# Optimization experiments

Hardware: AMD Instinct MI355X
Metric: run time of the kernel (lower is better)

The kernel has to match this reference:

```python
import jax, jax.numpy as jnp
import numpy as np

DIM = 2048
NUM_HEADS = 16
HEAD_DIM = DIM // NUM_HEADS
ROPE_BASE = 10000.0


def _rotate_half(t):
    t1, t2 = jnp.split(t, 2, axis=-1)
    return jnp.concatenate([-t2, t1], axis=-1)


def _rope_sin_cos(seq_len):
    # fp32 angles, matching RoPE1D
    inv_freq = 1.0 / (ROPE_BASE ** (jnp.arange(0, HEAD_DIM, 2, dtype=jnp.float32) / HEAD_DIM))
    freqs = jnp.arange(seq_len, dtype=jnp.float32)[:, None] * inv_freq[None, :]  # [S, hd/2]
    angles = jnp.concatenate([freqs, freqs], axis=-1)  # [S, hd]
    return jnp.sin(angles), jnp.cos(angles)


def setup_inputs() -> dict:
    key = jax.random.key(0)
    ks = jax.random.split(key, 5)
    B, S = 2, 2048
    x = jax.random.normal(ks[0], (B, S, DIM), dtype=jnp.float32)
    scale = 1.0 / np.sqrt(DIM)
    W_qkv = jax.random.normal(ks[1], (DIM, 3 * DIM), dtype=jnp.float32) * scale
    b_qkv = jnp.zeros((3 * DIM,), dtype=jnp.float32)
    W_proj = jax.random.normal(ks[2], (DIM, DIM), dtype=jnp.float32) * scale
    b_proj = jnp.zeros((DIM,), dtype=jnp.float32)
    return {"x": x, "W_qkv": W_qkv, "b_qkv": b_qkv, "W_proj": W_proj, "b_proj": b_proj}


def reference(x, W_qkv, b_qkv, W_proj, b_proj):
    B, S, D = x.shape
    H, hd = NUM_HEADS, HEAD_DIM
    qkv = x @ W_qkv + b_qkv  # [B, S, 3D]
    qkv = qkv.reshape(B, S, 3, H, hd)
    q, k, v = qkv[:, :, 0], qkv[:, :, 1], qkv[:, :, 2]  # [B, S, H, hd]
    q, k, v = (t.transpose(0, 2, 1, 3) for t in (q, k, v))  # [B, H, S, hd]
    sin, cos = _rope_sin_cos(S)  # [S, hd]
    sin = sin[None, None]
    cos = cos[None, None]
    q = q * cos + _rotate_half(q) * sin
    k = k * cos + _rotate_half(k) * sin
    # scaled dot-product attention (non-causal, no mask, no dropout)
    scale = 1.0 / np.sqrt(hd).astype(np.float32)
    scores = jnp.einsum("bhqd,bhkd->bhqk", q, k) * scale
    attn = jax.nn.softmax(scores, axis=-1)
    out = jnp.einsum("bhqk,bhkd->bhqd", attn, v)  # [B, H, S, hd]
    out = out.transpose(0, 2, 1, 3).reshape(B, S, D)
    return out @ W_proj + b_proj
```

## Files before the change

### kernel.cpp

```cpp
#include <hip/hip_runtime.h>


typedef __attribute__((ext_vector_type(4))) float  f32x4;
typedef __attribute__((ext_vector_type(8))) short  short8;
typedef __attribute__((ext_vector_type(4))) float  fv4;
typedef __attribute__((ext_vector_type(4))) unsigned short us4;

#define MFMA16(accv, av, bv) \
  asm volatile("v_mfma_f32_16x16x32_bf16 %0, %1, %2, %0" : "+v"(accv) : "v"(av), "v"(bv))

__device__ __forceinline__ unsigned short f2bf(float f) {
  unsigned int u = __float_as_uint(f);
  u += 0x7fffu + ((u >> 16) & 1u);
  return (unsigned short)(u >> 16);
}

__device__ __forceinline__ void gl_lds16(const void* g, void* l) {
  __builtin_amdgcn_global_load_lds((const __attribute__((address_space(1))) void*)g,
                                   (__attribute__((address_space(3))) void*)l, 16, 0, 0);
}

__global__ void cvt_f32_bf16(const float* __restrict__ in,
                             unsigned short* __restrict__ out, int n4) {
  int i = blockIdx.x * blockDim.x + threadIdx.x;
  int stride = gridDim.x * blockDim.x;
  for (; i < n4; i += stride) {
    fv4 v = ((const fv4*)in)[i];
    us4 o;
    o[0] = f2bf(v[0]); o[1] = f2bf(v[1]); o[2] = f2bf(v[2]); o[3] = f2bf(v[3]);
    ((us4*)out)[i] = o;
  }
}

__global__ void transpose_cvt(const float* __restrict__ in,
                              unsigned short* __restrict__ out, int R, int C) {
  __shared__ float tile[32][33];
  int c0 = blockIdx.x * 32, r0 = blockIdx.y * 32;
  int tx = threadIdx.x, ty = threadIdx.y;
#pragma unroll
  for (int i = 0; i < 4; i++)
    tile[ty + i * 8][tx] = in[(size_t)(r0 + ty + i * 8) * C + c0 + tx];
  __syncthreads();
#pragma unroll
  for (int i = 0; i < 4; i++)
    out[(size_t)(c0 + ty + i * 8) * R + r0 + tx] = f2bf(tile[tx][ty + i * 8]);
}

__global__ __launch_bounds__(512, 2) void qkv_gemm(
    const unsigned short* __restrict__ A,
    const unsigned short* __restrict__ Bt,
    const float* __restrict__ bias,
    unsigned short* __restrict__ Qo,
    unsigned short* __restrict__ Ko,
    unsigned short* __restrict__ Vo)
{
  __shared__ __align__(16) unsigned short SH[65536];

  const int NWG = 384;
  int bid = blockIdx.x;
  int nid = (bid & 7) * (NWG / 8) + (bid >> 3);
  int by = nid / 24, bx = nid - by * 24;

  int tid = threadIdx.x;
  int wv = tid >> 6, lane = tid & 63;
  int wr = wv >> 2, wc = wv & 3;
  int g = lane >> 4, c = lane & 15;

  int m0 = by * 256, n0 = bx * 256;

  int lh = wc >> 1, jj = wc & 1;
  int F[4];
#pragma unroll
  for (int n = 0; n < 4; n++) F[n] = 8 * lh + 2 * jj + (n & 1) + ((n >> 1) << 2);

  f32x4 acc[8][4];
#pragma unroll
  for (int m = 0; m < 8; m++)
#pragma unroll
    for (int n = 0; n < 4; n++)
#pragma unroll
      for (int r = 0; r < 4; r++) acc[m][n][r] = 0.f;

  auto stage = [&](int buf, int kt) {
    int k0 = kt * 32;
    unsigned short* Ad = SH + buf * 8192;
    unsigned short* Bd = SH + 32768 + buf * 8192;
#pragma unroll
    for (int p = 0; p < 2; p++) {
      int e = p * 512 + tid;
      int row = e >> 2, sl = (e & 3) ^ ((row >> 1) & 3);
      gl_lds16(A  + (size_t)(m0 + row) * 2048 + k0 + sl * 8,
               Ad + p * 4096 + wv * 512);
      gl_lds16(Bt + (size_t)(n0 + row) * 2048 + k0 + sl * 8,
               Bd + p * 4096 + wv * 512);
    }
  };

  stage(0, 0); stage(1, 1); stage(2, 2);

  for (int t = 0; t < 64; t++) {
    if (t < 62)       asm volatile("s_waitcnt vmcnt(8)" ::: "memory");
    else if (t == 62) asm volatile("s_waitcnt vmcnt(4)" ::: "memory");
    else              asm volatile("s_waitcnt vmcnt(0)" ::: "memory");
    __builtin_amdgcn_s_barrier();

    const unsigned short* Ab = SH + (t & 3) * 8192;
    const unsigned short* Bb = SH + 32768 + (t & 3) * 8192;

    short8 af[8], bfv[4];
#pragma unroll
    for (int m = 0; m < 8; m++) {
      int row = wr * 128 + m * 16 + c;
      af[m] = *(const short8*)(Ab + row * 32 + ((g ^ ((row >> 1) & 3)) << 3));
    }
#pragma unroll
    for (int n = 0; n < 4; n++) {
      int row = F[n] * 16 + c;
      bfv[n] = *(const short8*)(Bb + row * 32 + ((g ^ ((row >> 1) & 3)) << 3));
    }

    if (t < 61) stage((t + 3) & 3, t + 3);

    __builtin_amdgcn_s_setprio(1);
#pragma unroll
    for (int m = 0; m < 8; m++)
#pragma unroll
      for (int n = 0; n < 4; n++)
        MFMA16(acc[m][n], af[m], bfv[n]);
    __builtin_amdgcn_s_setprio(0);
  }

  int sel = bx >> 3;
  int bxl = bx & 7;
  int b = by >> 3;

  float biasv[4];
#pragma unroll
  for (int n = 0; n < 4; n++) biasv[n] = bias[n0 + F[n] * 16 + c];

  if (sel == 2) {
    __syncthreads();
    unsigned short* Vs = SH;
#pragma unroll
    for (int m = 0; m < 8; m++)
#pragma unroll
      for (int n = 0; n < 4; n++) {
        int dp = F[n] * 16 + c;
        int sb = wr * 128 + m * 16 + 4 * g;
        us4 pk;
#pragma unroll
        for (int r = 0; r < 4; r++) pk[r] = f2bf(acc[m][n][r] + biasv[n]);
        *(us4*)(Vs + dp * 256 + (sb ^ ((dp & 7) << 3))) = pk;
      }
    __syncthreads();
#pragma unroll
    for (int it = 0; it < 16; it++) {
      int u = it * 512 + tid;
      int dp = u >> 5, ch = u & 31;
      short8 val = *(const short8*)(Vs + dp * 256 + ((ch ^ (dp & 7)) << 3));
      int head = bxl * 2 + (dp >> 7), d = dp & 127;
      int sg = (by & 7) * 256 + ch * 8;
      *(short8*)(Vo + ((size_t)((b * 16 + head) * 128 + d)) * 2048 + sg) = val;
    }
  } else {
    unsigned short* outp = (sel == 0) ? Qo : Ko;
    float qscale = (sel == 0) ? (0.08838834764831845f * 1.44269504088896340736f) : 1.0f;
    int head = bxl * 2 + lh;
    float invf[2];
#pragma unroll
    for (int j = 0; j < 2; j++)
      invf[j] = __expf(-(float)((2 * jj + j) * 16 + c) * 0.14391156831212787f);
#pragma unroll
    for (int m = 0; m < 8; m++) {
#pragma unroll
      for (int j = 0; j < 2; j++) {
        int dlo = (2 * jj + j) * 16 + c;
#pragma unroll
        for (int r = 0; r < 4; r++) {
          int s_seq = (by & 7) * 256 + wr * 128 + m * 16 + 4 * g + r;
          float ang = (float)s_seq * invf[j];
          float sn, cs;
          __sincosf(ang, &sn, &cs);
          float vlo = acc[m][j][r]     + biasv[j];
          float vhi = acc[m][j + 2][r] + biasv[j + 2];
          float rlo = (vlo * cs - vhi * sn) * qscale;
          float rhi = (vhi * cs + vlo * sn) * qscale;
          size_t base = ((size_t)((b * 16 + head) * 2048 + s_seq)) * 128;
          outp[base + dlo]      = f2bf(rlo);
          outp[base + dlo + 64] = f2bf(rhi);
        }
      }
    }
  }
}

__global__ __launch_bounds__(256, 2) void attn_kernel(
    const unsigned short* __restrict__ Qi,
    const unsigned short* __restrict__ Ki,
    const unsigned short* __restrict__ Vi,
    unsigned short* __restrict__ X2)
{
  __shared__ __align__(16) unsigned short Kl[2][64 * 128];
  __shared__ __align__(16) unsigned short Vl[2][128 * 64];
  __shared__ __align__(16) unsigned short Pl[4][32 * 64];

  int bid = blockIdx.x;
  int nid = (bid & 7) * 64 + (bid >> 3);
  int bh = nid >> 4, qblk = nid & 15;
  int tid = threadIdx.x, wv = tid >> 6, lane = tid & 63;
  int g = lane >> 4, c = lane & 15;

  const unsigned short* Kg = Ki + (size_t)bh * 2048 * 128;
  const unsigned short* Vg = Vi + (size_t)bh * 128 * 2048;
  const unsigned short* Qb = Qi + ((size_t)bh * 2048 + qblk * 128 + wv * 32) * 128;

  short8 qf[2][4];
#pragma unroll
  for (int qt = 0; qt < 2; qt++)
#pragma unroll
    for (int dc = 0; dc < 4; dc++)
      qf[qt][dc] = *(const short8*)(Qb + (size_t)(qt * 16 + c) * 128 + dc * 32 + g * 8);

  f32x4 accO[2][8];
#pragma unroll
  for (int qt = 0; qt < 2; qt++)
#pragma unroll
    for (int nt = 0; nt < 8; nt++)
#pragma unroll
      for (int r = 0; r < 4; r++) accO[qt][nt][r] = 0.f;
  float m_run[2] = {-3.0e38f, -3.0e38f};
  float l_run[2] = {0.f, 0.f};

  auto stage = [&](int bsel, int t0) {
#pragma unroll
    for (int j = 0; j < 4; j++) {
      int e = j * 256 + tid;
      int s = e >> 4, sl = e & 15;
      gl_lds16(Kg + (size_t)(t0 + s) * 128 + ((sl ^ (s & 7)) * 8),
               &Kl[bsel][(size_t)(j * 256 + wv * 64) * 8]);
    }
#pragma unroll
    for (int j = 0; j < 4; j++) {
      int e = j * 256 + tid;
      int d = e >> 3, sl = e & 7;
      gl_lds16(Vg + (size_t)d * 2048 + t0 + ((sl ^ (d & 7)) * 8),
               &Vl[bsel][(size_t)(j * 256 + wv * 64) * 8]);
    }
  };

  stage(0, 0);
  __syncthreads();

  int cur = 0;
  for (int t = 0; t < 32; t++) {
    if (t < 31) stage(cur ^ 1, (t + 1) * 64);

    const unsigned short* Kt_ = &Kl[cur][0];
    const unsigned short* Vt_ = &Vl[cur][0];
    unsigned short* Pw = &Pl[wv][0];

    f32x4 sc[2][4];
#pragma unroll
    for (int qt = 0; qt < 2; qt++)
#pragma unroll
      for (int kt = 0; kt < 4; kt++)
#pragma unroll
        for (int r = 0; r < 4; r++) sc[qt][kt][r] = 0.f;

#pragma unroll
    for (int kt = 0; kt < 4; kt++) {
      short8 kf[4];
#pragma unroll
      for (int dc = 0; dc < 4; dc++)
        kf[dc] = *(const short8*)(Kt_ + (size_t)(kt * 16 + c) * 128 +
                                  (((dc * 4 + g) ^ (c & 7)) * 8));
      __builtin_amdgcn_s_setprio(1);
#pragma unroll
      for (int dc = 0; dc < 4; dc++) {
        MFMA16(sc[0][kt], kf[dc], qf[0][dc]);
        MFMA16(sc[1][kt], kf[dc], qf[1][dc]);
      }
      __builtin_amdgcn_s_setprio(0);
    }

    float mx[2];
#pragma unroll
    for (int qt = 0; qt < 2; qt++) {
      f32x4 mv = sc[qt][0];
#pragma unroll
      for (int kt = 1; kt < 4; kt++)
#pragma unroll
        for (int r = 0; r < 4; r++) mv[r] = fmaxf(mv[r], sc[qt][kt][r]);
      float m0 = fmaxf(fmaxf(mv[0], mv[1]), fmaxf(mv[2], mv[3]));
      m0 = fmaxf(m0, __shfl_xor(m0, 16));
      m0 = fmaxf(m0, __shfl_xor(m0, 32));
      mx[qt] = m0;
    }
    if (__any((mx[0] > m_run[0]) || (mx[1] > m_run[1]))) {
#pragma unroll
      for (int qt = 0; qt < 2; qt++) {
        float mnew = fmaxf(m_run[qt], mx[qt]);
        float al = __builtin_exp2f(m_run[qt] - mnew);
        l_run[qt] *= al;
        m_run[qt] = mnew;
#pragma unroll
        for (int r = 0; r < 4; r++) {
          float alr = __shfl(al, 4 * g + r);
#pragma unroll
          for (int nt = 0; nt < 8; nt++) accO[qt][nt][r] *= alr;
        }
      }
    }
#pragma unroll
    for (int qt = 0; qt < 2; qt++) {
      float rs = 0.f;
#pragma unroll
      for (int kt = 0; kt < 4; kt++) {
        float p0 = __builtin_exp2f(sc[qt][kt][0] - m_run[qt]);
        float p1 = __builtin_exp2f(sc[qt][kt][1] - m_run[qt]);
        float p2 = __builtin_exp2f(sc[qt][kt][2] - m_run[qt]);
        float p3 = __builtin_exp2f(sc[qt][kt][3] - m_run[qt]);
        rs += (p0 + p1) + (p2 + p3);
        unsigned int lo, hi;
        asm("v_cvt_pk_bf16_f32 %0, %1, %2" : "=v"(lo) : "v"(p0), "v"(p1));
        asm("v_cvt_pk_bf16_f32 %0, %1, %2" : "=v"(hi) : "v"(p2), "v"(p3));
        uint2 pk; pk.x = lo; pk.y = hi;
        *(uint2*)(Pw + (size_t)(qt * 16 + c) * 64 +
                  (((kt * 2 + (g >> 1)) ^ (c & 7)) * 8) + (g & 1) * 4) = pk;
      }
      rs += __shfl_xor(rs, 16);
      rs += __shfl_xor(rs, 32);
      l_run[qt] += rs;
    }

    short8 pa[2][2];
#pragma unroll
    for (int qt = 0; qt < 2; qt++)
#pragma unroll
      for (int kc = 0; kc < 2; kc++)
        pa[qt][kc] = *(const short8*)(Pw + (size_t)(qt * 16 + c) * 64 +
                                      (((kc * 4 + g) ^ (c & 7)) * 8));
#pragma unroll
    for (int nt = 0; nt < 8; nt++) {
      short8 vf0 = *(const short8*)(Vt_ + (size_t)(nt * 16 + c) * 64 +
                                    ((g ^ (c & 7)) * 8));
      short8 vf1 = *(const short8*)(Vt_ + (size_t)(nt * 16 + c) * 64 +
                                    (((4 + g) ^ (c & 7)) * 8));
      __builtin_amdgcn_s_setprio(1);
      MFMA16(accO[0][nt], pa[0][0], vf0);
      MFMA16(accO[1][nt], pa[1][0], vf0);
      MFMA16(accO[0][nt], pa[0][1], vf1);
      MFMA16(accO[1][nt], pa[1][1], vf1);
      __builtin_amdgcn_s_setprio(0);
    }

    __syncthreads();
    cur ^= 1;
  }

  float rl[2] = {1.f / l_run[0], 1.f / l_run[1]};
  int b = bh >> 4, h = bh & 15;
  size_t rowbase = (size_t)b * 2048 + qblk * 128 + wv * 32;
#pragma unroll
  for (int qt = 0; qt < 2; qt++)
#pragma unroll
    for (int r = 0; r < 4; r++) {
      float rr = __shfl(rl[qt], 4 * g + r);
      size_t row = rowbase + qt * 16 + 4 * g + r;
#pragma unroll
      for (int nt = 0; nt < 8; nt++)
        X2[row * 2048 + h * 128 + nt * 16 + c] = f2bf(accO[qt][nt][r] * rr);
    }
}

__global__ __launch_bounds__(512, 2) void proj_gemm(
    const unsigned short* __restrict__ A,
    const unsigned short* __restrict__ Bt,
    const float* __restrict__ bias,
    float* __restrict__ Co)
{
  __shared__ __align__(16) unsigned short SH[49152];

  int bid = blockIdx.x;
  int nid = (bid & 7) * 32 + (bid >> 3);
  int by = nid >> 4, bx = nid & 15;

  int tid = threadIdx.x;
  int wv = tid >> 6, lane = tid & 63;
  int wr = wv >> 1, wc = wv & 1;
  int g = lane >> 4, c = lane & 15;

  int m0 = by * 256, n0 = bx * 128;

  f32x4 acc[4][4];
#pragma unroll
  for (int m = 0; m < 4; m++)
#pragma unroll
    for (int n = 0; n < 4; n++)
#pragma unroll
      for (int r = 0; r < 4; r++) acc[m][n][r] = 0.f;

  auto stage = [&](int buf, int kt) {
    int k0 = kt * 32;
    unsigned short* Ad = SH + buf * 8192;
    unsigned short* Bd = SH + 32768 + buf * 4096;
#pragma unroll
    for (int p = 0; p < 2; p++) {
      int e = p * 512 + tid;
      int row = e >> 2, sl = (e & 3) ^ ((row >> 1) & 3);
      gl_lds16(A + (size_t)(m0 + row) * 2048 + k0 + sl * 8,
               Ad + p * 4096 + wv * 512);
    }
    {
      int e = tid;
      int row = e >> 2, sl = (e & 3) ^ ((row >> 1) & 3);
      gl_lds16(Bt + (size_t)(n0 + row) * 2048 + k0 + sl * 8,
               Bd + wv * 512);
    }
  };

  stage(0, 0); stage(1, 1); stage(2, 2);

  for (int t = 0; t < 64; t++) {
    if (t < 62)       asm volatile("s_waitcnt vmcnt(6)" ::: "memory");
    else if (t == 62) asm volatile("s_waitcnt vmcnt(3)" ::: "memory");
    else              asm volatile("s_waitcnt vmcnt(0)" ::: "memory");
    __builtin_amdgcn_s_barrier();

    const unsigned short* Ab = SH + (t & 3) * 8192;
    const unsigned short* Bb = SH + 32768 + (t & 3) * 4096;

    short8 af[4], bfv[4];
#pragma unroll
    for (int m = 0; m < 4; m++) {
      int row = wr * 64 + m * 16 + c;
      af[m] = *(const short8*)(Ab + row * 32 + ((g ^ ((row >> 1) & 3)) << 3));
    }
#pragma unroll
    for (int n = 0; n < 4; n++) {
      int row = (wc * 4 + n) * 16 + c;
      bfv[n] = *(const short8*)(Bb + row * 32 + ((g ^ ((row >> 1) & 3)) << 3));
    }

    if (t < 61) stage((t + 3) & 3, t + 3);

    __builtin_amdgcn_s_setprio(1);
#pragma unroll
    for (int m = 0; m < 4; m++)
#pragma unroll
      for (int n = 0; n < 4; n++)
        MFMA16(acc[m][n], af[m], bfv[n]);
    __builtin_amdgcn_s_setprio(0);
  }

#pragma unroll
  for (int m = 0; m < 4; m++)
#pragma unroll
    for (int n = 0; n < 4; n++)
#pragma unroll
      for (int r = 0; r < 4; r++) {
        int row = m0 + wr * 64 + m * 16 + 4 * g + r;
        int col = n0 + wc * 64 + n * 16 + c;
        Co[(size_t)row * 2048 + col] = acc[m][n][r] + bias[col];
      }
}

extern "C" void kernel_launch(void* const* d_in, const int* in_sizes, int n_in,
                              void* d_out, int out_size, void* d_ws, size_t ws_size,
                              hipStream_t stream) {
  (void)in_sizes; (void)n_in; (void)out_size; (void)ws_size;

  const float* x      = (const float*)d_in[0];
  const float* W_qkv  = (const float*)d_in[1];
  const float* b_qkv  = (const float*)d_in[2];
  const float* W_proj = (const float*)d_in[3];
  const float* b_proj = (const float*)d_in[4];
  float* out = (float*)d_out;

  unsigned short* xb     = (unsigned short*)d_ws;
  unsigned short* wqkvT  = xb     + 8388608;
  unsigned short* wprojT = wqkvT  + 12582912;
  unsigned short* Qb     = wprojT + 4194304;
  unsigned short* Kb     = Qb     + 8388608;
  unsigned short* Vtb    = Kb     + 8388608;
  unsigned short* x2     = Vtb    + 8388608;

  cvt_f32_bf16<<<2048, 256, 0, stream>>>(x, xb, 8388608 / 4);
  transpose_cvt<<<dim3(192, 64), dim3(32, 8), 0, stream>>>(W_qkv, wqkvT, 2048, 6144);
  transpose_cvt<<<dim3(64, 64),  dim3(32, 8), 0, stream>>>(W_proj, wprojT, 2048, 2048);
  qkv_gemm<<<384, 512, 0, stream>>>(xb, wqkvT, b_qkv, Qb, Kb, Vtb);
  attn_kernel<<<512, 256, 0, stream>>>(Qb, Kb, Vtb, x2);
  proj_gemm<<<256, 512, 0, stream>>>(x2, wprojT, b_proj, out);
}
```

Baseline: 399.7 us.

## Lazily rescale softmax with threshold, defer row reductions, precompute LDS offsets

The online-softmax rescale now fires only when a lane's local score max exceeds the running max by more than 8 (in log2 units). The running max is wave-reduced only inside that rescale path, and the per-lane row-sum shuffles move from every tile to a single reduction in the epilogue. Swizzled LDS read and write addresses for K, V and P are precomputed once as XOR-able offsets instead of being recomputed in each iteration. This cuts cross-lane shuffles, exp and rescale work in the main loop, at the cost of unnormalized P values up to 2^8 being stored in bf16.

```diff
diff --git a/kernel.cpp b/kernel.cpp
--- a/kernel.cpp
+++ b/kernel.cpp
@@ -231,6 +231,17 @@
   float m_run[2] = {-3.0e38f, -3.0e38f};
   float l_run[2] = {0.f, 0.f};
 
+  int cb2  = (c >> 2) & 1;
+  int gl2  = g ^ (c & 3);
+  int koff  = c * 128 + gl2 * 8 + cb2 * 32;
+  int koffx = koff ^ 32;
+  int voff  = c * 64 + gl2 * 8 + cb2 * 32;
+  int voffx = voff ^ 32;
+  int pwoff = c * 64 + (((g >> 1) ^ (c & 1)) * 8) + (g & 1) * 4 + (((c >> 1) & 3) * 16);
+  int proff  = c * 64 + gl2 * 8 + cb2 * 32;
+  int proffx = proff ^ 32;
+  unsigned short* Pw = &Pl[wv][0];
+
   auto stage = [&](int bsel, int t0) {
 #pragma unroll
     for (int j = 0; j < 4; j++) {
@@ -257,7 +268,6 @@
 
     const unsigned short* Kt_ = &Kl[cur][0];
     const unsigned short* Vt_ = &Vl[cur][0];
-    unsigned short* Pw = &Pl[wv][0];
 
     f32x4 sc[2][4];
 #pragma unroll
@@ -270,10 +280,10 @@
 #pragma unroll
     for (int kt = 0; kt < 4; kt++) {
       short8 kf[4];
-#pragma unroll
-      for (int dc = 0; dc < 4; dc++)
-        kf[dc] = *(const short8*)(Kt_ + (size_t)(kt * 16 + c) * 128 +
-                                  (((dc * 4 + g) ^ (c & 7)) * 8));
+      kf[0] = *(const short8*)(Kt_ + koff  + kt * 2048);
+      kf[1] = *(const short8*)(Kt_ + koffx + kt * 2048);
+      kf[2] = *(const short8*)(Kt_ + koff  + 64 + kt * 2048);
+      kf[3] = *(const short8*)(Kt_ + koffx + 64 + kt * 2048);
       __builtin_amdgcn_s_setprio(1);
 #pragma unroll
       for (int dc = 0; dc < 4; dc++) {
@@ -291,15 +301,16 @@
       for (int kt = 1; kt < 4; kt++)
 #pragma unroll
         for (int r = 0; r < 4; r++) mv[r] = fmaxf(mv[r], sc[qt][kt][r]);
-      float m0 = fmaxf(fmaxf(mv[0], mv[1]), fmaxf(mv[2], mv[3]));
-      m0 = fmaxf(m0, __shfl_xor(m0, 16));
-      m0 = fmaxf(m0, __shfl_xor(m0, 32));
-      mx[qt] = m0;
-    }
-    if (__any((mx[0] > m_run[0]) || (mx[1] > m_run[1]))) {
+      mx[qt] = fmaxf(fmaxf(mv[0], mv[1]), fmaxf(mv[2], mv[3]));
+    }
+    int grow = (mx[0] > m_run[0] + 8.f) | (mx[1] > m_run[1] + 8.f);
+    if (__any(grow)) {
 #pragma unroll
       for (int qt = 0; qt < 2; qt++) {
-        float mnew = fmaxf(m_run[qt], mx[qt]);
+        float mm = mx[qt];
+        mm = fmaxf(mm, __shfl_xor(mm, 16));
+        mm = fmaxf(mm, __shfl_xor(mm, 32));
+        float mnew = fmaxf(m_run[qt], mm);
         float al = __builtin_exp2f(m_run[qt] - mnew);
         l_run[qt] *= al;
         m_run[qt] = mnew;
@@ -325,27 +336,21 @@
         asm("v_cvt_pk_bf16_f32 %0, %1, %2" : "=v"(lo) : "v"(p0), "v"(p1));
         asm("v_cvt_pk_bf16_f32 %0, %1, %2" : "=v"(hi) : "v"(p2), "v"(p3));
         uint2 pk; pk.x = lo; pk.y = hi;
-        *(uint2*)(Pw + (size_t)(qt * 16 + c) * 64 +
-                  (((kt * 2 + (g >> 1)) ^ (c & 7)) * 8) + (g & 1) * 4) = pk;
+        *(uint2*)(Pw + (pwoff ^ (kt * 16)) + qt * 1024) = pk;
       }
-      rs += __shfl_xor(rs, 16);
-      rs += __shfl_xor(rs, 32);
       l_run[qt] += rs;
     }
 
     short8 pa[2][2];
 #pragma unroll
-    for (int qt = 0; qt < 2; qt++)
-#pragma unroll
-      for (int kc = 0; kc < 2; kc++)
-        pa[qt][kc] = *(const short8*)(Pw + (size_t)(qt * 16 + c) * 64 +
-                                      (((kc * 4 + g) ^ (c & 7)) * 8));
+    for (int qt = 0; qt < 2; qt++) {
+      pa[qt][0] = *(const short8*)(Pw + proff  + qt * 1024);
+      pa[qt][1] = *(const short8*)(Pw + proffx + qt * 1024);
+    }
 #pragma unroll
     for (int nt = 0; nt < 8; nt++) {
-      short8 vf0 = *(const short8*)(Vt_ + (size_t)(nt * 16 + c) * 64 +
-                                    ((g ^ (c & 7)) * 8));
-      short8 vf1 = *(const short8*)(Vt_ + (size_t)(nt * 16 + c) * 64 +
-                                    (((4 + g) ^ (c & 7)) * 8));
+      short8 vf0 = *(const short8*)(Vt_ + voff  + nt * 1024);
+      short8 vf1 = *(const short8*)(Vt_ + voffx + nt * 1024);
       __builtin_amdgcn_s_setprio(1);
       MFMA16(accO[0][nt], pa[0][0], vf0);
       MFMA16(accO[1][nt], pa[1][0], vf0);
@@ -358,7 +363,14 @@
     cur ^= 1;
   }
 
-  float rl[2] = {1.f / l_run[0], 1.f / l_run[1]};
+  float rl[2];
+#pragma unroll
+  for (int qt = 0; qt < 2; qt++) {
+    float l = l_run[qt];
+    l += __shfl_xor(l, 16);
+    l += __shfl_xor(l, 32);
+    rl[qt] = 1.0f / l;
+  }
   int b = bh >> 4, h = bh & 15;
   size_t rowbase = (size_t)b * 2048 + qblk * 128 + wv * 32;
 #pragma unroll
```

Result: no change. 392.7 us (-1.8%).
